# Performance work log

Hardware: AMD Instinct MI355X
Metric: run time of the kernel (lower is better)

Reference implementation:

```python
import jax, jax.numpy as jnp
import numpy as np

N_NODES = 50000


def gcn_conv(x, edge_index, W, b):
    """PyG GCNConv: add self-loops, symmetric deg^{-1/2} norm, W then aggregate."""
    n = x.shape[0]
    loops = jnp.arange(n, dtype=edge_index.dtype)
    src = jnp.concatenate([edge_index[0], loops])  # message sources
    dst = jnp.concatenate([edge_index[1], loops])  # aggregation targets
    h = x @ W  # [N, out_dim] -- transform before gather (PyG order)
    deg = jax.ops.segment_sum(jnp.ones_like(dst, dtype=h.dtype), dst, num_segments=n)
    dinv = jnp.where(deg > 0, jax.lax.rsqrt(jnp.maximum(deg, 1.0)), 0.0)
    norm = dinv[src] * dinv[dst]  # [E+N]
    msg = h[src] * norm[:, None]  # gather + normalize
    out = jax.ops.segment_sum(msg, dst, num_segments=n)  # scatter-add
    return out + b


def setup_inputs() -> dict:
    key = jax.random.key(0)
    k1, k2, k3, k4, k5 = jax.random.split(key, 5)
    N, E, D_IN, D_H, D_OUT = N_NODES, 800000, 128, 256, 16
    x = jax.random.normal(k1, (N, D_IN), dtype=jnp.float32)
    edge_index = jax.random.randint(k2, (2, E), 0, N, dtype=jnp.int64)
    s1 = 1.0 / np.sqrt(D_IN)
    s2 = 1.0 / np.sqrt(D_H)
    W1 = jax.random.uniform(k3, (D_IN, D_H), jnp.float32, -s1, s1)
    b1 = jnp.zeros((D_H,), jnp.float32)
    W2 = jax.random.uniform(k4, (D_H, D_OUT), jnp.float32, -s2, s2)
    b2 = jnp.zeros((D_OUT,), jnp.float32)
    return {"x": x, "edge_index": edge_index, "W1": W1, "b1": b1, "W2": W2, "b2": b2}


def reference(x, edge_index, W1, b1, W2, b2):
    h = jax.nn.relu(gcn_conv(x, edge_index, W1, b1))
    # dropout is identity in eval mode
    logits = gcn_conv(h, edge_index, W2, b2)
    return jax.nn.log_softmax(logits, axis=-1)
```

## Files before the change

### kernel.cpp

```cpp
#include <hip/hip_runtime.h>
#include <math.h>

typedef unsigned int uint;
typedef unsigned short u16;
typedef short short8 __attribute__((ext_vector_type(8)));
typedef float floatx4 __attribute__((ext_vector_type(4)));

union U4S8 { uint4 u; short8 s; };

#define CAPC 64
#define BPB  4096


__device__ __forceinline__ float blo(uint u) { return __uint_as_float(u << 16); }
__device__ __forceinline__ float bhi(uint u) { return __uint_as_float(u & 0xffff0000u); }
__device__ __forceinline__ uint pack_bf16(float a, float b) {
    uint ua = __float_as_uint(a), ub = __float_as_uint(b);
    ua = (ua + 0x7fffu + ((ua >> 16) & 1u)) >> 16;
    ub = (ub + 0x7fffu + ((ub >> 16) & 1u)) >> 16;
    return ua | (ub << 16);
}
__device__ __forceinline__ unsigned short rb16(float f) {
    uint u = __float_as_uint(f);
    return (unsigned short)((u + 0x7fffu + ((u >> 16) & 1u)) >> 16);
}
__device__ __forceinline__ int us(short v) { return (int)(unsigned short)v; }


__global__ void k_init(const float* __restrict__ W1, const float* __restrict__ W2,
                       uint* __restrict__ W1t, uint* __restrict__ W2t) {
    int i = blockIdx.x * 256 + threadIdx.x;
    if (i < 16384) {
        int nn = i >> 6, kd = i & 63;
        W1t[i] = pack_bf16(W1[(size_t)(2 * kd) * 256 + nn], W1[(size_t)(2 * kd + 1) * 256 + nn]);
    } else if (i < 16384 + 2048) {
        int j = i - 16384;
        int o = j >> 7, kd = j & 127;
        W2t[j] = pack_bf16(W2[(size_t)(2 * kd) * 16 + o], W2[(size_t)(2 * kd + 1) * 16 + o]);
    }
}


__global__ __launch_bounds__(256) void k_binhist(const int* __restrict__ ei, int E, int nblk,
                                                 uint* __restrict__ blkhist) {
    __shared__ uint hist[256];
    int blk = blockIdx.x, tid = threadIdx.x;
    hist[tid] = 0;
    __syncthreads();
    int base = blk * BPB;
    int end = min(base + BPB, E);
    for (int i = base + tid; i < end; i += 256) {
        int t = ei[E + i];
        atomicAdd(&hist[t >> 8], 1u);
    }
    __syncthreads();
    blkhist[(size_t)tid * nblk + blk] = hist[tid];
}

__global__ __launch_bounds__(256) void k_binscan1(const uint* __restrict__ blkhist, int nblk,
                                                  uint* __restrict__ blkoff,
                                                  uint* __restrict__ bintot) {
    __shared__ uint s[256];
    int b = blockIdx.x, tid = threadIdx.x;
    uint v = (tid < nblk) ? blkhist[(size_t)b * nblk + tid] : 0u;
    s[tid] = v;
    __syncthreads();
    #pragma unroll
    for (int off = 1; off < 256; off <<= 1) {
        uint t = (tid >= off) ? s[tid - off] : 0u;
        __syncthreads();
        s[tid] += t;
        __syncthreads();
    }
    if (tid < nblk) blkoff[(size_t)b * nblk + tid] = s[tid] - v;
    if (tid == 255) bintot[b] = s[255];
}

__global__ __launch_bounds__(256) void k_binscan2(const uint* __restrict__ bintot, int nbins,
                                                  uint* __restrict__ binoff) {
    __shared__ uint s[256];
    int tid = threadIdx.x;
    uint v = (tid < nbins) ? bintot[tid] : 0u;
    s[tid] = v;
    __syncthreads();
    #pragma unroll
    for (int off = 1; off < 256; off <<= 1) {
        uint t = (tid >= off) ? s[tid - off] : 0u;
        __syncthreads();
        s[tid] += t;
        __syncthreads();
    }
    binoff[tid] = s[tid] - v;
}

__global__ __launch_bounds__(256) void k_binscatter(const int* __restrict__ ei, int E, int nblk,
                                                    const uint* __restrict__ binoff,
                                                    const uint* __restrict__ blkoff,
                                                    uint* __restrict__ ebin) {
    __shared__ uint cnt[256];
    int blk = blockIdx.x, tid = threadIdx.x;
    cnt[tid] = 0;
    __syncthreads();
    int base = blk * BPB;
    int end = min(base + BPB, E);
    for (int i = base + tid; i < end; i += 256) {
        int s = ei[i], t = ei[E + i];
        int bin = t >> 8;
        uint local = atomicAdd(&cnt[bin], 1u);
        uint pos = binoff[bin] + blkoff[(size_t)bin * nblk + blk] + local;
        ebin[pos] = ((uint)t << 16) | (uint)s;
    }
}

__global__ __launch_bounds__(256) void k_binbucket(const uint* __restrict__ ebin,
                                                   const uint* __restrict__ binoff,
                                                   const uint* __restrict__ bintot,
                                                   u16* __restrict__ colc, int* __restrict__ degc,
                                                   float* __restrict__ dinv, int n) {
    __shared__ uint lbw[256 * 32];
    __shared__ uint lc[256];
    u16* lb = (u16*)lbw;
    int b = blockIdx.x, tid = threadIdx.x;
    lc[tid] = 0;
    __syncthreads();
    uint base = binoff[b], m = bintot[b];
    for (uint i = tid; i < m; i += 256) {
        uint e = ebin[base + i];
        int tl = (int)((e >> 16) & 255u);
        uint c = atomicAdd(&lc[tl], 1u);
        if (c < (uint)CAPC) lb[tl * CAPC + c] = (u16)(e & 0xffffu);
    }
    __syncthreads();
    int node0 = b << 8;
    int node = node0 + tid;
    if (node < n) {
        uint c = lc[tid];
        degc[node] = (int)min(c, (uint)CAPC);
        dinv[node] = rsqrtf((float)c + 1.0f);
    }
    uint* colw = (uint*)colc;
    for (int idx = tid; idx < 256 * 32; idx += 256) {
        int nd = node0 + (idx >> 5);
        if (nd < n) colw[(size_t)nd * 32 + (idx & 31)] = lbw[idx];
    }
}


__global__ void k_scale_cast(const float* __restrict__ dinv,
                             const float2* __restrict__ x2,
                             uint* __restrict__ xsb, int total) {
    int j = blockIdx.x * 256 + threadIdx.x;
    if (j >= total) return;
    int row = j >> 6;
    float di = dinv[row];
    float2 v = x2[j];
    xsb[j] = pack_bf16(v.x * di, v.y * di);
}


__global__ __launch_bounds__(256) void k_agg_csr128(
    const int* __restrict__ degc, const u16* __restrict__ colc,
    const float* __restrict__ dinv, const uint* __restrict__ xsb,
    uint* __restrict__ outb, int n)
{
    int node = (blockIdx.x * 256 + threadIdx.x) >> 6;
    int lane = threadIdx.x & 63;
    if (node >= n) return;
    float di = dinv[node];
    int deg = min(degc[node], CAPC);
    const u16* bucket = colc + (size_t)node * CAPC;
    uint u = xsb[(size_t)node * 64 + lane];
    float ax = blo(u), ay = bhi(u);
    int j = 0;
    for (; j + 8 <= deg; j += 8) {
        U4S8 bi; bi.u = *(const uint4*)&bucket[j];
        uint u0 = xsb[(size_t)us(bi.s[0]) * 64 + lane];
        uint u1 = xsb[(size_t)us(bi.s[1]) * 64 + lane];
        uint u2 = xsb[(size_t)us(bi.s[2]) * 64 + lane];
        uint u3 = xsb[(size_t)us(bi.s[3]) * 64 + lane];
        uint u4 = xsb[(size_t)us(bi.s[4]) * 64 + lane];
        uint u5 = xsb[(size_t)us(bi.s[5]) * 64 + lane];
        uint u6 = xsb[(size_t)us(bi.s[6]) * 64 + lane];
        uint u7 = xsb[(size_t)us(bi.s[7]) * 64 + lane];
        ax += blo(u0) + blo(u1) + blo(u2) + blo(u3) + blo(u4) + blo(u5) + blo(u6) + blo(u7);
        ay += bhi(u0) + bhi(u1) + bhi(u2) + bhi(u3) + bhi(u4) + bhi(u5) + bhi(u6) + bhi(u7);
    }
    for (; j < deg; ++j) {
        uint uu = xsb[(size_t)bucket[j] * 64 + lane];
        ax += blo(uu); ay += bhi(uu);
    }
    outb[(size_t)node * 64 + lane] = pack_bf16(ax * di, ay * di);
}


__global__ __launch_bounds__(256) void k_gemm_mfma(
    const uint* __restrict__ Ab,
    const uint* __restrict__ W1t,
    const float* __restrict__ b1,
    const uint* __restrict__ W2t,
    const float* __restrict__ dinv,
    float* __restrict__ H2, int M)
{
    __shared__ uint Alds[64 * 68];
    __shared__ uint Hlds[64 * 132];

    const int t    = threadIdx.x;
    const int mb   = blockIdx.x * 64;
    const int wv   = t >> 6;
    const int lane = t & 63;
    const int c    = lane & 15;
    const int q    = lane >> 4;

    #pragma unroll
    for (int it = 0; it < 4; ++it) {
        int i = it * 256 + t;
        int r = i >> 4, cc = i & 15;
        int gr = mb + r;
        uint4 v = make_uint4(0u, 0u, 0u, 0u);
        if (gr < M) v = ((const uint4*)Ab)[(size_t)gr * 16 + cc];
        *(uint4*)&Alds[r * 68 + cc * 4] = v;
    }
    __syncthreads();

    floatx4 acc[4][4];
    #pragma unroll
    for (int i = 0; i < 4; ++i)
        #pragma unroll
        for (int jj = 0; jj < 4; ++jj) acc[i][jj] = (floatx4)0.f;

    #pragma unroll
    for (int kk = 0; kk < 4; ++kk) {
        U4S8 af[4];
        #pragma unroll
        for (int mt = 0; mt < 4; ++mt)
            af[mt].u = *(const uint4*)&Alds[(mt * 16 + c) * 68 + kk * 16 + q * 4];
        #pragma unroll
        for (int nt = 0; nt < 4; ++nt) {
            int n = wv * 64 + nt * 16 + c;
            U4S8 bf;
            bf.u = ((const uint4*)W1t)[(size_t)n * 16 + kk * 4 + q];
            #pragma unroll
            for (int mt = 0; mt < 4; ++mt)
                acc[mt][nt] = __builtin_amdgcn_mfma_f32_16x16x32_bf16(
                    af[mt].s, bf.s, acc[mt][nt], 0, 0, 0);
        }
    }

    float b1v[4];
    #pragma unroll
    for (int nt = 0; nt < 4; ++nt) b1v[nt] = b1[wv * 64 + nt * 16 + c];

    unsigned short* hs = (unsigned short*)Hlds;
    #pragma unroll
    for (int mt = 0; mt < 4; ++mt)
        #pragma unroll
        for (int nt = 0; nt < 4; ++nt)
            #pragma unroll
            for (int r = 0; r < 4; ++r) {
                float hv = fmaxf(acc[mt][nt][r] + b1v[nt], 0.f);
                int row = mt * 16 + q * 4 + r;
                int colc2 = wv * 64 + nt * 16 + c;
                hs[row * 264 + colc2] = rb16(hv);
            }
    __syncthreads();

    floatx4 acc2 = (floatx4)0.f;
    #pragma unroll
    for (int kk = 0; kk < 8; ++kk) {
        U4S8 av, bv;
        av.u = *(const uint4*)&Hlds[(wv * 16 + c) * 132 + kk * 16 + q * 4];
        bv.u = ((const uint4*)W2t)[(size_t)c * 32 + kk * 4 + q];
        acc2 = __builtin_amdgcn_mfma_f32_16x16x32_bf16(av.s, bv.s, acc2, 0, 0, 0);
    }
    #pragma unroll
    for (int r = 0; r < 4; ++r) {
        int gr = mb + wv * 16 + q * 4 + r;
        if (gr < M) H2[(size_t)gr * 16 + c] = acc2[r] * dinv[gr];
    }
}


__global__ __launch_bounds__(256) void k_agg_csr16_lsm(
    const int* __restrict__ degc, const u16* __restrict__ colc,
    const float* __restrict__ dinv, const float* __restrict__ h2s,
    const float* __restrict__ b2, float* __restrict__ out, int n)
{
    int node = (blockIdx.x * 256 + threadIdx.x) >> 4;
    int lane = threadIdx.x & 15;
    if (node >= n) return;
    float di = dinv[node];
    int deg = min(degc[node], CAPC);
    const u16* bucket = colc + (size_t)node * CAPC;
    float acc = h2s[(size_t)node * 16 + lane];
    int j = 0;
    for (; j + 8 <= deg; j += 8) {
        U4S8 bi; bi.u = *(const uint4*)&bucket[j];
        float v0 = h2s[(size_t)us(bi.s[0]) * 16 + lane];
        float v1 = h2s[(size_t)us(bi.s[1]) * 16 + lane];
        float v2 = h2s[(size_t)us(bi.s[2]) * 16 + lane];
        float v3 = h2s[(size_t)us(bi.s[3]) * 16 + lane];
        float v4 = h2s[(size_t)us(bi.s[4]) * 16 + lane];
        float v5 = h2s[(size_t)us(bi.s[5]) * 16 + lane];
        float v6 = h2s[(size_t)us(bi.s[6]) * 16 + lane];
        float v7 = h2s[(size_t)us(bi.s[7]) * 16 + lane];
        acc += v0 + v1 + v2 + v3 + v4 + v5 + v6 + v7;
    }
    for (; j < deg; ++j) acc += h2s[(size_t)bucket[j] * 16 + lane];
    acc = acc * di + b2[lane];
    float m = acc;
    #pragma unroll
    for (int msk = 1; msk < 16; msk <<= 1) m = fmaxf(m, __shfl_xor(m, msk, 16));
    float ex = __expf(acc - m);
    float ssum = ex;
    #pragma unroll
    for (int msk = 1; msk < 16; msk <<= 1) ssum += __shfl_xor(ssum, msk, 16);
    out[(size_t)node * 16 + lane] = acc - m - __logf(ssum);
}


extern "C" void kernel_launch(void* const* d_in, const int* in_sizes, int n_in,
                              void* d_out, int out_size, void* d_ws, size_t ws_size,
                              hipStream_t stream) {
    const float* x  = (const float*)d_in[0];
    const int*   ei = (const int*)d_in[1];
    const float* W1 = (const float*)d_in[2];
    const float* b1 = (const float*)d_in[3];
    const float* W2 = (const float*)d_in[4];
    const float* b2 = (const float*)d_in[5];
    float* out = (float*)d_out;

    const int N = in_sizes[0] / 128;
    const int E = in_sizes[1] / 2;

    const int NBINS = (N + 255) >> 8;
    const int NBLK  = (E + BPB - 1) / BPB;

    float* ws      = (float*)d_ws;
    float* dinv    = ws;
    int*   degc    = (int*)(ws + 51200);
    uint*  binoff  = (uint*)(ws + 102400);
    uint*  bintot  = (uint*)(ws + 102656);
    uint*  blkhist = (uint*)(ws + 102912);
    uint*  blkoff  = (uint*)(ws + 154112);
    uint*  ebin    = (uint*)(ws + 205312);
    u16*   colc    = (u16*)(ws + 1005312);
    uint*  xsb     = (uint*)(ws + 2605312);
    float* h2s     = (float*)(ws + 2605312);
    uint*  aggb    = (uint*)(ws + 5805312);
    uint*  W1t     = (uint*)(ws + 9005312);
    uint*  W2t     = (uint*)(ws + 9021696);

    k_init      <<<72, 256, 0, stream>>>(W1, W2, W1t, W2t);
    k_binhist   <<<NBLK, 256, 0, stream>>>(ei, E, NBLK, blkhist);
    k_binscan1  <<<NBINS, 256, 0, stream>>>(blkhist, NBLK, blkoff, bintot);
    k_binscan2  <<<1, 256, 0, stream>>>(bintot, NBINS, binoff);
    k_binscatter<<<NBLK, 256, 0, stream>>>(ei, E, NBLK, binoff, blkoff, ebin);
    k_binbucket <<<NBINS, 256, 0, stream>>>(ebin, binoff, bintot, colc, degc, dinv, N);

    k_scale_cast<<<(N * 64 + 255) / 256, 256, 0, stream>>>(dinv, (const float2*)x, xsb, N * 64);
    k_agg_csr128<<<(N * 64 + 255) / 256, 256, 0, stream>>>(degc, colc, dinv, xsb, aggb, N);
    k_gemm_mfma <<<(N + 63) / 64, 256, 0, stream>>>(aggb, W1t, b1, W2t, dinv, h2s, N);
    k_agg_csr16_lsm<<<(N * 16 + 255) / 256, 256, 0, stream>>>(degc, colc, dinv, h2s, b2, out, N);
}
```

Baseline: 189.1 us.

## Fuse preprocessing kernels and aggregate layer-1 features directly inside GEMM

```diff
diff --git a/kernel.cpp b/kernel.cpp
--- a/kernel.cpp
+++ b/kernel.cpp
@@ -27,35 +27,34 @@
 __device__ __forceinline__ int us(short v) { return (int)(unsigned short)v; }
 
 
-__global__ void k_init(const float* __restrict__ W1, const float* __restrict__ W2,
-                       uint* __restrict__ W1t, uint* __restrict__ W2t) {
-    int i = blockIdx.x * 256 + threadIdx.x;
-    if (i < 16384) {
-        int nn = i >> 6, kd = i & 63;
-        W1t[i] = pack_bf16(W1[(size_t)(2 * kd) * 256 + nn], W1[(size_t)(2 * kd + 1) * 256 + nn]);
-    } else if (i < 16384 + 2048) {
-        int j = i - 16384;
-        int o = j >> 7, kd = j & 127;
-        W2t[j] = pack_bf16(W2[(size_t)(2 * kd) * 16 + o], W2[(size_t)(2 * kd + 1) * 16 + o]);
-    }
-}
-
-
-__global__ __launch_bounds__(256) void k_binhist(const int* __restrict__ ei, int E, int nblk,
-                                                 uint* __restrict__ blkhist) {
+__global__ __launch_bounds__(256) void k_init_hist(
+    const int* __restrict__ ei, int E, int nblk, uint* __restrict__ blkhist,
+    const float* __restrict__ W1, const float* __restrict__ W2,
+    uint* __restrict__ W1t, uint* __restrict__ W2t)
+{
     __shared__ uint hist[256];
     int blk = blockIdx.x, tid = threadIdx.x;
-    hist[tid] = 0;
-    __syncthreads();
-    int base = blk * BPB;
-    int end = min(base + BPB, E);
-    for (int i = base + tid; i < end; i += 256) {
-        int t = ei[E + i];
-        atomicAdd(&hist[t >> 8], 1u);
-    }
-    __syncthreads();
-    blkhist[(size_t)tid * nblk + blk] = hist[tid];
-}
+    if (blk < nblk) {
+        hist[tid] = 0;
+        __syncthreads();
+        int base = blk * BPB, end = min(base + BPB, E);
+        for (int i = base + tid; i < end; i += 256)
+            atomicAdd(&hist[ei[E + i] >> 8], 1u);
+        __syncthreads();
+        blkhist[(size_t)tid * nblk + blk] = hist[tid];
+    } else {
+        int i = (blk - nblk) * 256 + tid;
+        if (i < 16384) {
+            int nn = i >> 6, kd = i & 63;
+            W1t[i] = pack_bf16(W1[(size_t)(2 * kd) * 256 + nn], W1[(size_t)(2 * kd + 1) * 256 + nn]);
+        } else if (i < 16384 + 2048) {
+            int j = i - 16384;
+            int o = j >> 7, kd = j & 127;
+            W2t[j] = pack_bf16(W2[(size_t)(2 * kd) * 16 + o], W2[(size_t)(2 * kd + 1) * 16 + o]);
+        }
+    }
+}
+
 
 __global__ __launch_bounds__(256) void k_binscan1(const uint* __restrict__ blkhist, int nblk,
                                                   uint* __restrict__ blkoff,
@@ -76,54 +75,67 @@
     if (tid == 255) bintot[b] = s[255];
 }
 
-__global__ __launch_bounds__(256) void k_binscan2(const uint* __restrict__ bintot, int nbins,
-                                                  uint* __restrict__ binoff) {
+
+__global__ __launch_bounds__(256) void k_binscatter(const int* __restrict__ ei, int E,
+                                                    int nblk, int nbins,
+                                                    const uint* __restrict__ bintot,
+                                                    const uint* __restrict__ blkoff,
+                                                    uint* __restrict__ ebin) {
     __shared__ uint s[256];
-    int tid = threadIdx.x;
+    __shared__ uint off[256];
+    __shared__ uint cnt[256];
+    int blk = blockIdx.x, tid = threadIdx.x;
     uint v = (tid < nbins) ? bintot[tid] : 0u;
     s[tid] = v;
     __syncthreads();
     #pragma unroll
-    for (int off = 1; off < 256; off <<= 1) {
-        uint t = (tid >= off) ? s[tid - off] : 0u;
+    for (int o = 1; o < 256; o <<= 1) {
+        uint t = (tid >= o) ? s[tid - o] : 0u;
         __syncthreads();
         s[tid] += t;
         __syncthreads();
     }
-    binoff[tid] = s[tid] - v;
-}
-
-__global__ __launch_bounds__(256) void k_binscatter(const int* __restrict__ ei, int E, int nblk,
-                                                    const uint* __restrict__ binoff,
-                                                    const uint* __restrict__ blkoff,
-                                                    uint* __restrict__ ebin) {
-    __shared__ uint cnt[256];
-    int blk = blockIdx.x, tid = threadIdx.x;
+    uint bo = (tid < nbins) ? blkoff[(size_t)tid * nblk + blk] : 0u;
+    off[tid] = (s[tid] - v) + bo;
     cnt[tid] = 0;
     __syncthreads();
-    int base = blk * BPB;
-    int end = min(base + BPB, E);
+    int base = blk * BPB, end = min(base + BPB, E);
     for (int i = base + tid; i < end; i += 256) {
-        int s = ei[i], t = ei[E + i];
-        int bin = t >> 8;
+        int sv = ei[i], tv = ei[E + i];
+        int bin = tv >> 8;
         uint local = atomicAdd(&cnt[bin], 1u);
-        uint pos = binoff[bin] + blkoff[(size_t)bin * nblk + blk] + local;
-        ebin[pos] = ((uint)t << 16) | (uint)s;
-    }
-}
-
-__global__ __launch_bounds__(256) void k_binbucket(const uint* __restrict__ ebin,
-                                                   const uint* __restrict__ binoff,
-                                                   const uint* __restrict__ bintot,
-                                                   u16* __restrict__ colc, int* __restrict__ degc,
-                                                   float* __restrict__ dinv, int n) {
+        ebin[off[bin] + local] = ((uint)tv << 16) | (uint)sv;
+    }
+}
+
+
+__global__ __launch_bounds__(256) void k_binbucket_scale(
+    const uint* __restrict__ ebin, const uint* __restrict__ bintot, int nbins,
+    u16* __restrict__ colc, int* __restrict__ degc, float* __restrict__ dinv,
+    const float2* __restrict__ x2, uint* __restrict__ xsb, int n)
+{
     __shared__ uint lbw[256 * 32];
     __shared__ uint lc[256];
+    __shared__ uint s[256];
+    __shared__ float ldi[256];
     u16* lb = (u16*)lbw;
     int b = blockIdx.x, tid = threadIdx.x;
+
+    uint v = (tid < nbins) ? bintot[tid] : 0u;
+    s[tid] = v;
+    __syncthreads();
+    #pragma unroll
+    for (int o = 1; o < 256; o <<= 1) {
+        uint t = (tid >= o) ? s[tid - o] : 0u;
+        __syncthreads();
+        s[tid] += t;
+        __syncthreads();
+    }
+    uint m = bintot[b];
+    uint base = s[b] - m;
     lc[tid] = 0;
     __syncthreads();
-    uint base = binoff[b], m = bintot[b];
+
     for (uint i = tid; i < m; i += 256) {
         uint e = ebin[base + i];
         int tl = (int)((e >> 16) & 255u);
@@ -131,74 +143,39 @@
         if (c < (uint)CAPC) lb[tl * CAPC + c] = (u16)(e & 0xffffu);
     }
     __syncthreads();
+
     int node0 = b << 8;
     int node = node0 + tid;
+    float di = rsqrtf((float)lc[tid] + 1.0f);
+    ldi[tid] = di;
     if (node < n) {
-        uint c = lc[tid];
-        degc[node] = (int)min(c, (uint)CAPC);
-        dinv[node] = rsqrtf((float)c + 1.0f);
+        degc[node] = (int)min(lc[tid], (uint)CAPC);
+        dinv[node] = di;
     }
     uint* colw = (uint*)colc;
     for (int idx = tid; idx < 256 * 32; idx += 256) {
         int nd = node0 + (idx >> 5);
         if (nd < n) colw[(size_t)nd * 32 + (idx & 31)] = lbw[idx];
     }
-}
-
-
-__global__ void k_scale_cast(const float* __restrict__ dinv,
-                             const float2* __restrict__ x2,
-                             uint* __restrict__ xsb, int total) {
-    int j = blockIdx.x * 256 + threadIdx.x;
-    if (j >= total) return;
-    int row = j >> 6;
-    float di = dinv[row];
-    float2 v = x2[j];
-    xsb[j] = pack_bf16(v.x * di, v.y * di);
-}
-
-
-__global__ __launch_bounds__(256) void k_agg_csr128(
+    __syncthreads();
+
+    for (int idx = tid; idx < 256 * 64; idx += 256) {
+        int nd = node0 + (idx >> 6);
+        if (nd < n) {
+            float dd = ldi[idx >> 6];
+            float2 xv = x2[(size_t)nd * 64 + (idx & 63)];
+            xsb[(size_t)nd * 64 + (idx & 63)] = pack_bf16(xv.x * dd, xv.y * dd);
+        }
+    }
+}
+
+
+__global__ __launch_bounds__(256) void k_gemm_agg(
     const int* __restrict__ degc, const u16* __restrict__ colc,
     const float* __restrict__ dinv, const uint* __restrict__ xsb,
-    uint* __restrict__ outb, int n)
-{
-    int node = (blockIdx.x * 256 + threadIdx.x) >> 6;
-    int lane = threadIdx.x & 63;
-    if (node >= n) return;
-    float di = dinv[node];
-    int deg = min(degc[node], CAPC);
-    const u16* bucket = colc + (size_t)node * CAPC;
-    uint u = xsb[(size_t)node * 64 + lane];
-    float ax = blo(u), ay = bhi(u);
-    int j = 0;
-    for (; j + 8 <= deg; j += 8) {
-        U4S8 bi; bi.u = *(const uint4*)&bucket[j];
-        uint u0 = xsb[(size_t)us(bi.s[0]) * 64 + lane];
-        uint u1 = xsb[(size_t)us(bi.s[1]) * 64 + lane];
-        uint u2 = xsb[(size_t)us(bi.s[2]) * 64 + lane];
-        uint u3 = xsb[(size_t)us(bi.s[3]) * 64 + lane];
-        uint u4 = xsb[(size_t)us(bi.s[4]) * 64 + lane];
-        uint u5 = xsb[(size_t)us(bi.s[5]) * 64 + lane];
-        uint u6 = xsb[(size_t)us(bi.s[6]) * 64 + lane];
-        uint u7 = xsb[(size_t)us(bi.s[7]) * 64 + lane];
-        ax += blo(u0) + blo(u1) + blo(u2) + blo(u3) + blo(u4) + blo(u5) + blo(u6) + blo(u7);
-        ay += bhi(u0) + bhi(u1) + bhi(u2) + bhi(u3) + bhi(u4) + bhi(u5) + bhi(u6) + bhi(u7);
-    }
-    for (; j < deg; ++j) {
-        uint uu = xsb[(size_t)bucket[j] * 64 + lane];
-        ax += blo(uu); ay += bhi(uu);
-    }
-    outb[(size_t)node * 64 + lane] = pack_bf16(ax * di, ay * di);
-}
-
-
-__global__ __launch_bounds__(256) void k_gemm_mfma(
-    const uint* __restrict__ Ab,
     const uint* __restrict__ W1t,
     const float* __restrict__ b1,
     const uint* __restrict__ W2t,
-    const float* __restrict__ dinv,
     float* __restrict__ H2, int M)
 {
     __shared__ uint Alds[64 * 68];
@@ -211,14 +188,37 @@
     const int c    = lane & 15;
     const int q    = lane >> 4;
 
-    #pragma unroll
-    for (int it = 0; it < 4; ++it) {
-        int i = it * 256 + t;
-        int r = i >> 4, cc = i & 15;
+    for (int i = 0; i < 16; ++i) {
+        int r = wv * 16 + i;
         int gr = mb + r;
-        uint4 v = make_uint4(0u, 0u, 0u, 0u);
-        if (gr < M) v = ((const uint4*)Ab)[(size_t)gr * 16 + cc];
-        *(uint4*)&Alds[r * 68 + cc * 4] = v;
+        uint outv = 0u;
+        if (gr < M) {
+            float di = dinv[gr];
+            int deg = min(degc[gr], CAPC);
+            const u16* bucket = colc + (size_t)gr * CAPC;
+            uint u = xsb[(size_t)gr * 64 + lane];
+            float ax = blo(u), ay = bhi(u);
+            int j = 0;
+            for (; j + 8 <= deg; j += 8) {
+                U4S8 bi; bi.u = *(const uint4*)&bucket[j];
+                uint u0 = xsb[(size_t)us(bi.s[0]) * 64 + lane];
+                uint u1 = xsb[(size_t)us(bi.s[1]) * 64 + lane];
+                uint u2 = xsb[(size_t)us(bi.s[2]) * 64 + lane];
+                uint u3 = xsb[(size_t)us(bi.s[3]) * 64 + lane];
+                uint u4 = xsb[(size_t)us(bi.s[4]) * 64 + lane];
+                uint u5 = xsb[(size_t)us(bi.s[5]) * 64 + lane];
+                uint u6 = xsb[(size_t)us(bi.s[6]) * 64 + lane];
+                uint u7 = xsb[(size_t)us(bi.s[7]) * 64 + lane];
+                ax += blo(u0) + blo(u1) + blo(u2) + blo(u3) + blo(u4) + blo(u5) + blo(u6) + blo(u7);
+                ay += bhi(u0) + bhi(u1) + bhi(u2) + bhi(u3) + bhi(u4) + bhi(u5) + bhi(u6) + bhi(u7);
+            }
+            for (; j < deg; ++j) {
+                uint uu = xsb[(size_t)bucket[j] * 64 + lane];
+                ax += blo(uu); ay += bhi(uu);
+            }
+            outv = pack_bf16(ax * di, ay * di);
+        }
+        Alds[r * 68 + lane] = outv;
     }
     __syncthreads();
 
@@ -338,27 +338,21 @@
     float* ws      = (float*)d_ws;
     float* dinv    = ws;
     int*   degc    = (int*)(ws + 51200);
-    uint*  binoff  = (uint*)(ws + 102400);
-    uint*  bintot  = (uint*)(ws + 102656);
-    uint*  blkhist = (uint*)(ws + 102912);
-    uint*  blkoff  = (uint*)(ws + 154112);
-    uint*  ebin    = (uint*)(ws + 205312);
-    u16*   colc    = (u16*)(ws + 1005312);
-    uint*  xsb     = (uint*)(ws + 2605312);
-    float* h2s     = (float*)(ws + 2605312);
-    uint*  aggb    = (uint*)(ws + 5805312);
-    uint*  W1t     = (uint*)(ws + 9005312);
-    uint*  W2t     = (uint*)(ws + 9021696);
-
-    k_init      <<<72, 256, 0, stream>>>(W1, W2, W1t, W2t);
-    k_binhist   <<<NBLK, 256, 0, stream>>>(ei, E, NBLK, blkhist);
+    uint*  bintot  = (uint*)(ws + 102400);
+    uint*  blkhist = (uint*)(ws + 102656);
+    uint*  blkoff  = (uint*)(ws + 168192);
+    uint*  ebin    = (uint*)(ws + 233728);
+    u16*   colc    = (u16*)(ws + 1033728);
+    uint*  xsb     = (uint*)(ws + 2633728);
+    float* h2s     = (float*)(ws + 5833728);
+    uint*  W1t     = (uint*)(ws + 6633728);
+    uint*  W2t     = (uint*)(ws + 6650112);
+
+    k_init_hist <<<NBLK + 72, 256, 0, stream>>>(ei, E, NBLK, blkhist, W1, W2, W1t, W2t);
     k_binscan1  <<<NBINS, 256, 0, stream>>>(blkhist, NBLK, blkoff, bintot);
-    k_binscan2  <<<1, 256, 0, stream>>>(bintot, NBINS, binoff);
-    k_binscatter<<<NBLK, 256, 0, stream>>>(ei, E, NBLK, binoff, blkoff, ebin);
-    k_binbucket <<<NBINS, 256, 0, stream>>>(ebin, binoff, bintot, colc, degc, dinv, N);
-
-    k_scale_cast<<<(N * 64 + 255) / 256, 256, 0, stream>>>(dinv, (const float2*)x, xsb, N * 64);
-    k_agg_csr128<<<(N * 64 + 255) / 256, 256, 0, stream>>>(degc, colc, dinv, xsb, aggb, N);
-    k_gemm_mfma <<<(N + 63) / 64, 256, 0, stream>>>(aggb, W1t, b1, W2t, dinv, h2s, N);
+    k_binscatter<<<NBLK, 256, 0, stream>>>(ei, E, NBLK, NBINS, bintot, blkoff, ebin);
+    k_binbucket_scale<<<NBINS, 256, 0, stream>>>(ebin, bintot, NBINS, colc, degc, dinv,
+                                                 (const float2*)x, xsb, N);
+    k_gemm_agg  <<<(N + 63) / 64, 256, 0, stream>>>(degc, colc, dinv, xsb, W1t, b1, W2t, h2s, N);
     k_agg_csr16_lsm<<<(N * 16 + 255) / 256, 256, 0, stream>>>(degc, colc, dinv, h2s, b2, out, N);
 }
```

Measured after the change: 273.2 us. +44.5%, slower.
